# Performance work log

Hardware: AMD Instinct MI355X
Metric: run time of the kernel (lower is better)

The kernel has to match this reference:

```python
import jax, jax.numpy as jnp
import numpy as np

B = 1024          # batch
L = 200           # max_len (history length)
DIM = 64          # args.dim
ITEM_NUM = 100000 # vocab; table has ITEM_NUM+1 rows, row 0 = padding
NEG = -1e15       # mask additive constant used by the original module


def setup_inputs() -> dict:
    key = jax.random.key(0)
    k1, k2, k3, k4, k5 = jax.random.split(key, 5)
    log_seqs = jax.random.randint(k1, (B, L), 0, ITEM_NUM + 1)          # item ids, 0 = pad
    pred = jax.random.randint(k2, (B, 1), 0, ITEM_NUM + 1)              # gather targets
    item_emb = jax.random.normal(k3, (ITEM_NUM + 1, DIM), jnp.float32) * 0.02
    item_emb = item_emb.at[0].set(0.0)                                  # padding_idx=0
    attn_key = jax.random.uniform(k4, (1, DIM), jnp.float32)            # self.key (torch.rand init)
    pos_emb = jax.random.normal(k5, (L, DIM), jnp.float32) * 0.02       # positional table
    return {"log_seqs": log_seqs, "pred": pred, "item_emb": item_emb,
            "attn_key": attn_key, "pos_emb": pos_emb}


def reference(log_seqs, pred, item_emb, attn_key, pos_emb):
    dim = item_emb.shape[1]
    mask = log_seqs != 0                                  # [B, L] True where valid
    # log2feats (model='P2MAMO', dropout p=0 -> identity)
    seqs = item_emb[log_seqs] * jnp.sqrt(jnp.float32(dim))  # [B, L, D]
    seqs = seqs + pos_emb[None, :, :]
    seqs = seqs * mask[..., None]                         # zero out padded positions
    # single-query dot-product attention pooling with learned key
    sim = jnp.einsum('bld,d->bl', seqs, attn_key[0])      # (q*k).sum(-1)
    sim = sim + jnp.where(mask, 0.0, NEG)                 # sim + (~mask)*-1e15
    attn = jax.nn.softmax(sim, axis=-1)                   # [B, L]
    Q = jnp.einsum('bld,bl->bd', seqs, attn)              # [B, D]
    # training path (isEval=False): full-vocab logits -> softmax -> gather
    logits = Q @ item_emb.T                               # [B, V+1]
    probs = jax.nn.softmax(logits, axis=-1)
    pos_logits = jnp.take_along_axis(probs, pred, axis=1) # [B, 1]
    return pos_logits
```

## Files before the change

kernel.cpp:

```cpp
#include <hip/hip_runtime.h>
#include <math.h>

#define B_TOT   1024
#define L_SEQ   200
#define DIM     64
#define VOCAB   100001
#define NEG_BIG (-1e15f)
#define SEQ_ST16 66
#define LOG2E   1.4426950408889634f
#define EB_SLACK_ROWS 512

typedef __bf16 bf16x8 __attribute__((ext_vector_type(8)));
typedef float  f32x4  __attribute__((ext_vector_type(4)));

static __device__ __forceinline__ float fast_exp2(float x) {
    return __builtin_amdgcn_exp2f(x);
}

__global__ __launch_bounds__(256) void pool_kernel(
    const int*   __restrict__ log_seqs,
    const float* __restrict__ item_emb,
    const float* __restrict__ attn_key,
    const float* __restrict__ pos_emb,
    float*       __restrict__ Q,
    __bf16*      __restrict__ Qb,
    __bf16*      __restrict__ Eb)
{
    const int b    = blockIdx.x;
    const int t    = threadIdx.x;
    const int wave = t >> 6;
    const int lane = t & 63;

    __shared__ unsigned short s_seq16[L_SEQ][SEQ_ST16];
    __shared__ float s_attn[L_SEQ];
    __shared__ float s_red[4];
    __shared__ float s_q[4][DIM];

    float sim = -INFINITY;
    if (t < L_SEQ) {
        const int id = log_seqs[(long)b * L_SEQ + t];
        if (id == 0) {
            sim = NEG_BIG;
            const ushort2 z = make_ushort2(0, 0);
            #pragma unroll
            for (int i = 0; i < DIM / 2; ++i)
                *(ushort2*)&s_seq16[t][2 * i] = z;
        } else {
            float acc = 0.f;
            const float4* e4 = (const float4*)(item_emb + (long)id * DIM);
            const float4* p4 = (const float4*)(pos_emb + t * DIM);
            #pragma unroll
            for (int i = 0; i < DIM / 4; ++i) {
                const float4 e = e4[i];
                const float4 p = p4[i];
                float4 f;
                f.x = fmaf(8.f, e.x, p.x);
                f.y = fmaf(8.f, e.y, p.y);
                f.z = fmaf(8.f, e.z, p.z);
                f.w = fmaf(8.f, e.w, p.w);
                const __bf16 h0 = (__bf16)f.x, h1 = (__bf16)f.y;
                const __bf16 h2 = (__bf16)f.z, h3 = (__bf16)f.w;
                ushort2 u0, u1;
                u0.x = __builtin_bit_cast(unsigned short, h0);
                u0.y = __builtin_bit_cast(unsigned short, h1);
                u1.x = __builtin_bit_cast(unsigned short, h2);
                u1.y = __builtin_bit_cast(unsigned short, h3);
                *(ushort2*)&s_seq16[t][4 * i]     = u0;
                *(ushort2*)&s_seq16[t][4 * i + 2] = u1;
                acc += f.x * attn_key[4*i+0] + f.y * attn_key[4*i+1]
                     + f.z * attn_key[4*i+2] + f.w * attn_key[4*i+3];
            }
            sim = acc;
        }
    }

    float m = sim;
    #pragma unroll
    for (int off = 32; off > 0; off >>= 1) m = fmaxf(m, __shfl_xor(m, off));
    if (lane == 0) s_red[wave] = m;
    __syncthreads();
    m = fmaxf(fmaxf(s_red[0], s_red[1]), fmaxf(s_red[2], s_red[3]));
    __syncthreads();

    float p = (t < L_SEQ) ? __expf(sim - m) : 0.f;
    if (t < L_SEQ) s_attn[t] = p;
    float ls = p;
    #pragma unroll
    for (int off = 32; off > 0; off >>= 1) ls += __shfl_xor(ls, off);
    if (lane == 0) s_red[wave] = ls;
    __syncthreads();
    const float inv = 1.0f / (s_red[0] + s_red[1] + s_red[2] + s_red[3]);

    float q = 0.f;
    const int l0 = wave * (L_SEQ / 4);
    #pragma unroll 2
    for (int l = l0; l < l0 + (L_SEQ / 4); ++l) {
        const unsigned int ui = (unsigned int)s_seq16[l][lane] << 16;
        q = fmaf(s_attn[l], __builtin_bit_cast(float, ui), q);
    }
    s_q[wave][lane] = q;
    __syncthreads();

    if (t < DIM) {
        const float qq = (s_q[0][t] + s_q[1][t] + s_q[2][t] + s_q[3][t]) * inv;
        Q[b * DIM + t]  = qq;
        Qb[b * DIM + t] = (__bf16)(qq * LOG2E);
    }

    {
        const long n8 = ((long)VOCAB * DIM) / 8;
        for (long g = (long)b * 256 + t; g < n8; g += (long)gridDim.x * 256) {
            const long i = g * 8;
            const float4 f0 = ((const float4*)(item_emb + i))[0];
            const float4 f1 = ((const float4*)(item_emb + i))[1];
            bf16x8 o;
            o[0] = (__bf16)f0.x; o[1] = (__bf16)f0.y; o[2] = (__bf16)f0.z; o[3] = (__bf16)f0.w;
            o[4] = (__bf16)f1.x; o[5] = (__bf16)f1.y; o[6] = (__bf16)f1.z; o[7] = (__bf16)f1.w;
            *(bf16x8*)(Eb + i) = o;
        }
    }
}

#define NC        256
#define NBG       8
#define VT_TOTAL  6251
#define VT_FULL   6250
#define VT_PER    25
#define STAGE_VT  8

__global__ __launch_bounds__(256) void logits_mfma(
    const __bf16* __restrict__ Eb,
    const __bf16* __restrict__ Qb,
    float*        __restrict__ partials)
{
    const int bid   = blockIdx.x;
    const int xcd   = bid & 7;
    const int idx   = bid >> 3;
    const int chunk = xcd + 8 * (idx >> 3);
    const int bg    = idx & 7;
    const int tid   = threadIdx.x;
    const int wave  = tid >> 6;
    const int lane  = tid & 63;
    const int r16   = lane & 15;
    const int hi    = lane >> 4;

    __shared__ char s_stage[STAGE_VT * 2048];

    bf16x8 a[2][2];
    #pragma unroll
    for (int t = 0; t < 2; ++t)
        #pragma unroll
        for (int s = 0; s < 2; ++s)
            a[t][s] = *(const bf16x8*)(Qb + ((bg*128 + (wave*2 + t)*16 + r16) * DIM) + s*32 + hi*8);

    const int vt0    = chunk * VT_PER;
    const int vt_end = min(vt0 + VT_PER, VT_TOTAL);
    const int nvt    = vt_end - vt0;
    const int nphase = nvt > 0 ? (nvt + STAGE_VT - 1) / STAGE_VT : 0;

    float ssum[2][4];
    #pragma unroll
    for (int t = 0; t < 2; ++t)
        #pragma unroll
        for (int r = 0; r < 4; ++r) ssum[t][r] = 0.f;

    const int rbase = r16 * 128;
    const int x0 = (hi * 16)        ^ ((r16 & 7) << 4);
    const int x1 = ((hi * 16) + 64) ^ ((r16 & 7) << 4);

    for (int ph = 0; ph < nphase; ++ph) {
        const int vtg0 = vt0 + ph * STAGE_VT;
        __syncthreads();
        {
            const __bf16* src = Eb + (size_t)vtg0 * 16 * DIM;
            bf16x8 v[4];
            #pragma unroll
            for (int k = 0; k < 4; ++k) {
                const int g = k * 256 + tid;
                v[k] = *(const bf16x8*)(src + (size_t)(g >> 3) * DIM + (g & 7) * 8);
            }
            #pragma unroll
            for (int k = 0; k < 4; ++k) {
                const int g    = k * 256 + tid;
                const int rowg = g >> 3;
                const int slot = g & 7;
                const int row  = rowg & 15;
                const int vl   = rowg >> 4;
                const int db   = vl * 2048 + row * 128 + ((slot * 16) ^ ((row & 7) << 4));
                *(bf16x8*)(s_stage + db) = v[k];
            }
        }
        __syncthreads();

        const int nv = min(STAGE_VT, vt_end - vtg0);
        for (int vl = 0; vl < nv; ++vl) {
            const char* vb = s_stage + vl * 2048 + rbase;
            const bf16x8 c0 = *(const bf16x8*)(vb + x0);
            const bf16x8 c1 = *(const bf16x8*)(vb + x1);
            const int vt_g = vtg0 + vl;
            if (vt_g < VT_FULL) {
                #pragma unroll
                for (int t = 0; t < 2; ++t) {
                    f32x4 acc = {0.f, 0.f, 0.f, 0.f};
                    acc = __builtin_amdgcn_mfma_f32_16x16x32_bf16(a[t][0], c0, acc, 0, 0, 0);
                    acc = __builtin_amdgcn_mfma_f32_16x16x32_bf16(a[t][1], c1, acc, 0, 0, 0);
                    #pragma unroll
                    for (int r = 0; r < 4; ++r) ssum[t][r] += fast_exp2(acc[r]);
                }
            } else {
                const bool valid = (vt_g * 16 + r16) < VOCAB;
                #pragma unroll
                for (int t = 0; t < 2; ++t) {
                    f32x4 acc = {0.f, 0.f, 0.f, 0.f};
                    acc = __builtin_amdgcn_mfma_f32_16x16x32_bf16(a[t][0], c0, acc, 0, 0, 0);
                    acc = __builtin_amdgcn_mfma_f32_16x16x32_bf16(a[t][1], c1, acc, 0, 0, 0);
                    #pragma unroll
                    for (int r = 0; r < 4; ++r) ssum[t][r] += valid ? fast_exp2(acc[r]) : 0.f;
                }
            }
        }
    }

    #pragma unroll
    for (int t = 0; t < 2; ++t)
        #pragma unroll
        for (int r = 0; r < 4; ++r) {
            float v = ssum[t][r];
            v += __shfl_xor(v, 1);
            v += __shfl_xor(v, 2);
            v += __shfl_xor(v, 4);
            v += __shfl_xor(v, 8);
            ssum[t][r] = v;
        }

    if (r16 == 0) {
        #pragma unroll
        for (int t = 0; t < 2; ++t)
            #pragma unroll
            for (int r = 0; r < 4; ++r) {
                const int row = bg * 128 + (wave*2 + t) * 16 + hi * 4 + r;
                partials[(size_t)chunk * B_TOT + row] = ssum[t][r];
            }
    }
}

__global__ __launch_bounds__(256) void finalize_kernel(
    const float* __restrict__ Q,
    const float* __restrict__ item_emb,
    const int*   __restrict__ pred,
    const float* __restrict__ partials,
    float*       __restrict__ out)
{
    const int b = blockIdx.x * 256 + threadIdx.x;

    float S = 0.f;
    for (int c = 0; c < NC; ++c)
        S += partials[(size_t)c * B_TOT + b];

    const int pv = pred[b];
    float acc = 0.f;
    const float4* e4 = (const float4*)(item_emb + (long)pv * DIM);
    const float4* q4 = (const float4*)(Q + b * DIM);
    #pragma unroll
    for (int i = 0; i < DIM / 4; ++i) {
        const float4 e = e4[i];
        const float4 q = q4[i];
        acc += e.x*q.x + e.y*q.y + e.z*q.z + e.w*q.w;
    }
    out[b] = __expf(acc) / S;
}

extern "C" void kernel_launch(void* const* d_in, const int* in_sizes, int n_in,
                              void* d_out, int out_size, void* d_ws, size_t ws_size,
                              hipStream_t stream)
{
    const int*   log_seqs = (const int*)  d_in[0];
    const int*   pred     = (const int*)  d_in[1];
    const float* item_emb = (const float*)d_in[2];
    const float* attn_key = (const float*)d_in[3];
    const float* pos_emb  = (const float*)d_in[4];
    float*       out      = (float*)d_out;

    char* ws = (char*)d_ws;
    const size_t eb_bytes = (size_t)(VOCAB + EB_SLACK_ROWS) * DIM * 2;
    __bf16* Eb       = (__bf16*)ws;
    __bf16* Qb       = (__bf16*)(ws + eb_bytes);
    float*  Qf       = (float*) (ws + eb_bytes + (size_t)B_TOT * DIM * 2);
    float*  partials = (float*) ((char*)Qf + (size_t)B_TOT * DIM * 4);

    pool_kernel<<<B_TOT, 256, 0, stream>>>(log_seqs, item_emb, attn_key, pos_emb, Qf, Qb, Eb);
    logits_mfma<<<NBG * NC, 256, 0, stream>>>(Eb, Qb, partials);
    finalize_kernel<<<B_TOT / 256, 256, 0, stream>>>(Qf, item_emb, pred, partials, out);
}
```

Measured before the change: 63.98 us.

## Coalesce embedding gather in pool kernel with 16 lanes per row

Reassigns the embedding gather in the pooling kernel so each row is read by 16 threads doing float4 loads, instead of one thread reading a full 256-byte row serially. Similarity partial sums are reduced with warp shuffles and staged through a new shared array before the softmax. This is meant to turn uncoalesced per-thread row reads into coalesced accesses and use all 256 threads. The cost is an extra barrier, extra shared memory, and shuffle work per row.

```diff
diff --git a/kernel.cpp b/kernel.cpp
--- a/kernel.cpp
+++ b/kernel.cpp
@@ -30,50 +30,53 @@
     const int t    = threadIdx.x;
     const int wave = t >> 6;
     const int lane = t & 63;
+    const int qw   = t >> 4;
+    const int ql   = t & 15;
 
     __shared__ unsigned short s_seq16[L_SEQ][SEQ_ST16];
+    __shared__ float s_sim[L_SEQ];
     __shared__ float s_attn[L_SEQ];
     __shared__ float s_red[4];
     __shared__ float s_q[4][DIM];
 
-    float sim = -INFINITY;
-    if (t < L_SEQ) {
-        const int id = log_seqs[(long)b * L_SEQ + t];
-        if (id == 0) {
-            sim = NEG_BIG;
-            const ushort2 z = make_ushort2(0, 0);
-            #pragma unroll
-            for (int i = 0; i < DIM / 2; ++i)
-                *(ushort2*)&s_seq16[t][2 * i] = z;
-        } else {
-            float acc = 0.f;
-            const float4* e4 = (const float4*)(item_emb + (long)id * DIM);
-            const float4* p4 = (const float4*)(pos_emb + t * DIM);
-            #pragma unroll
-            for (int i = 0; i < DIM / 4; ++i) {
-                const float4 e = e4[i];
-                const float4 p = p4[i];
+    {
+        const float4 key4 = ((const float4*)attn_key)[ql];
+        const int* seq_row = log_seqs + (long)b * L_SEQ;
+        #pragma unroll
+        for (int it = 0; it < 13; ++it) {
+            const int l = qw + it * 16;
+            if (l >= L_SEQ) break;
+            const int id = seq_row[l];
+            float acc;
+            if (id == 0) {
+                *(ushort4*)&s_seq16[l][4 * ql] = make_ushort4(0, 0, 0, 0);
+                acc = 0.f;
+            } else {
+                const float4 e = *(const float4*)(item_emb + (long)id * DIM + 4 * ql);
+                const float4 p = *(const float4*)(pos_emb + l * DIM + 4 * ql);
                 float4 f;
                 f.x = fmaf(8.f, e.x, p.x);
                 f.y = fmaf(8.f, e.y, p.y);
                 f.z = fmaf(8.f, e.z, p.z);
                 f.w = fmaf(8.f, e.w, p.w);
-                const __bf16 h0 = (__bf16)f.x, h1 = (__bf16)f.y;
-                const __bf16 h2 = (__bf16)f.z, h3 = (__bf16)f.w;
-                ushort2 u0, u1;
-                u0.x = __builtin_bit_cast(unsigned short, h0);
-                u0.y = __builtin_bit_cast(unsigned short, h1);
-                u1.x = __builtin_bit_cast(unsigned short, h2);
-                u1.y = __builtin_bit_cast(unsigned short, h3);
-                *(ushort2*)&s_seq16[t][4 * i]     = u0;
-                *(ushort2*)&s_seq16[t][4 * i + 2] = u1;
-                acc += f.x * attn_key[4*i+0] + f.y * attn_key[4*i+1]
-                     + f.z * attn_key[4*i+2] + f.w * attn_key[4*i+3];
-            }
-            sim = acc;
-        }
-    }
-
+                ushort4 u;
+                u.x = __builtin_bit_cast(unsigned short, (__bf16)f.x);
+                u.y = __builtin_bit_cast(unsigned short, (__bf16)f.y);
+                u.z = __builtin_bit_cast(unsigned short, (__bf16)f.z);
+                u.w = __builtin_bit_cast(unsigned short, (__bf16)f.w);
+                *(ushort4*)&s_seq16[l][4 * ql] = u;
+                acc = f.x * key4.x + f.y * key4.y + f.z * key4.z + f.w * key4.w;
+            }
+            acc += __shfl_xor(acc, 1);
+            acc += __shfl_xor(acc, 2);
+            acc += __shfl_xor(acc, 4);
+            acc += __shfl_xor(acc, 8);
+            if (ql == 0) s_sim[l] = (id == 0) ? NEG_BIG : acc;
+        }
+    }
+    __syncthreads();
+
+    float sim = (t < L_SEQ) ? s_sim[t] : -INFINITY;
     float m = sim;
     #pragma unroll
     for (int off = 32; off > 0; off >>= 1) m = fmaxf(m, __shfl_xor(m, off));
```

After: 62.00 us (median of 2 runs). 1.03x faster.
